# Optimization experiments

Hardware: AMD Instinct MI355X
Metric: run time of the kernel (lower is better)

Reference implementation:

```python
import jax, jax.numpy as jnp
import numpy as np

B, T, D, H = 2, 2048, 1024, 16
HD = D // H
ALPHA = HD ** -0.5
EPS = 1e-5


def setup_inputs() -> dict:
    key = jax.random.key(0)
    ks = jax.random.split(key, 8)
    x = jax.random.normal(ks[0], (B, T, D), dtype=jnp.float32)
    # additive causal mask: 0 where allowed, -inf where disallowed
    causal = jnp.triu(jnp.ones((T, T), dtype=bool), k=1)
    attention_mask = jnp.where(causal, -jnp.inf, 0.0).astype(jnp.float32)
    rab = jax.random.normal(ks[1], (1, H, T, T), dtype=jnp.float32) * 0.02
    W_in = jax.random.normal(ks[2], (D, 4 * D), dtype=jnp.float32) * (D ** -0.5)
    b_in = jnp.zeros((4 * D,), dtype=jnp.float32)
    W_out = jax.random.normal(ks[3], (D, D), dtype=jnp.float32) * (D ** -0.5)
    b_out = jnp.zeros((D,), dtype=jnp.float32)
    ln_w = jnp.ones((D,), dtype=jnp.float32)
    ln_b = jnp.zeros((D,), dtype=jnp.float32)
    return {"x": x, "attention_mask": attention_mask, "rab": rab,
            "W_in": W_in, "b_in": b_in, "W_out": W_out, "b_out": b_out,
            "ln_w": ln_w, "ln_b": ln_b}


def _heads(t):  # [B,T,D] -> [B,H,T,HD]
    return t.reshape(B, T, H, HD).transpose(0, 2, 1, 3)


def _layernorm(t, w, b):
    mu = jnp.mean(t, axis=-1, keepdims=True)
    var = jnp.mean(jnp.square(t - mu), axis=-1, keepdims=True)
    return (t - mu) * jax.lax.rsqrt(var + EPS) * w + b


def reference(x, attention_mask, rab, W_in, b_in, W_out, b_out, ln_w, ln_b):
    h = jax.nn.silu(x @ W_in + b_in)                      # [B,T,4D]
    U, V, Q, K = jnp.split(h, 4, axis=-1)
    Qh, Kh, Vh = _heads(Q), _heads(K), _heads(V)
    logits = jnp.einsum('bhqd,bhkd->bhqk', Qh, Kh) * ALPHA
    logits = logits + rab + attention_mask[None, None]    # [B,H,T,T]
    # allowed counts from the additive mask (0 == allowed)
    allowed = (attention_mask == 0).astype(jnp.float32)   # [T,T]
    denom = jnp.clip(jnp.sum(allowed, axis=-1, keepdims=True), 1.0)  # [T,1]
    logits_safe = jnp.where(jnp.isinf(logits) & (logits < 0), -1e9, logits)
    attn = jax.nn.silu(logits_safe) / denom[None, None]
    AV = jnp.einsum('bhqk,bhkd->bhqd', attn, Vh)
    AV = AV.transpose(0, 2, 1, 3).reshape(B, T, D)
    y = (_layernorm(AV, ln_w, ln_b) * U) @ W_out + b_out
    return y
```

## Files before the change

kernel.cpp:

```cpp
#include <hip/hip_runtime.h>

#define BATCH 2
#define TSEQ 2048
#define DIM 1024
#define NH 16
#define HDIM 64
#define MROWS (BATCH * TSEQ)

typedef __attribute__((ext_vector_type(4))) float f32x4;
typedef __attribute__((ext_vector_type(8))) short short8;

__device__ __forceinline__ unsigned short f2bf(float f) {
    union { float f; unsigned int u; } x; x.f = f;
    unsigned int r = x.u + 0x7fffu + ((x.u >> 16) & 1u);
    return (unsigned short)(r >> 16);
}

__device__ __forceinline__ float silu_f(float v) {
    return v * __builtin_amdgcn_rcpf(1.f + __expf(-v));
}

__device__ __forceinline__ void gl_lds16(const void* g, void* l) {
    __builtin_amdgcn_global_load_lds(
        (const __attribute__((address_space(1))) void*)g,
        (__attribute__((address_space(3))) void*)l, 16, 0, 0);
}

__device__ __forceinline__ short8 rd_swz(const unsigned short* base, int row, int chunk) {
    const char* b = (const char*)base;
    return *(const short8*)(b + row * 128 + (((chunk ^ (row & 7)) << 4)));
}

__global__ __launch_bounds__(256) void k_convert(const float* __restrict__ in,
                                                 unsigned short* __restrict__ out,
                                                 int n4) {
    int i = blockIdx.x * 256 + threadIdx.x;
    if (i < n4) {
        float4 v = ((const float4*)in)[i];
        union { unsigned short s[4]; uint2 u; } o;
        o.s[0] = f2bf(v.x); o.s[1] = f2bf(v.y); o.s[2] = f2bf(v.z); o.s[3] = f2bf(v.w);
        ((uint2*)out)[i] = o.u;
    }
}

__global__ __launch_bounds__(256) void k_transpose(const float* __restrict__ in,
                                                   unsigned short* __restrict__ out,
                                                   int R, int C) {
    __shared__ float tile[32][33];
    int tx = threadIdx.x, ty = threadIdx.y;
    int c0 = blockIdx.x * 32, r0 = blockIdx.y * 32;
    #pragma unroll
    for (int i = 0; i < 32; i += 8)
        tile[ty + i][tx] = in[(size_t)(r0 + ty + i) * C + c0 + tx];
    __syncthreads();
    #pragma unroll
    for (int i = 0; i < 32; i += 8)
        out[(size_t)(c0 + ty + i) * R + r0 + tx] = f2bf(tile[tx][ty + i]);
}

__device__ __forceinline__ void stage256(const unsigned short* __restrict__ A,
                                         const unsigned short* __restrict__ Bt,
                                         int row0, int col0, int k0,
                                         unsigned short* sAbuf, unsigned short* sBbuf,
                                         int tid) {
    #pragma unroll
    for (int q = 0; q < 4; ++q) {
        int c = tid + 512 * q;
        int rr = c >> 3;
        int kcs = (c & 7) ^ (rr & 7);
        gl_lds16(A + (size_t)(row0 + rr) * 1024 + k0 + kcs * 8, sAbuf + c * 8);
        gl_lds16(Bt + (size_t)(col0 + rr) * 1024 + k0 + kcs * 8, sBbuf + c * 8);
    }
}

__global__ __launch_bounds__(512, 2) void k_gemm1_256(
    const unsigned short* __restrict__ A, const unsigned short* __restrict__ Bt,
    const float* __restrict__ bias,
    float* __restrict__ outU, unsigned short* __restrict__ outVt,
    unsigned short* __restrict__ outQ, unsigned short* __restrict__ outK)
{
    __shared__ __align__(16) unsigned short sA[2][256 * 64];
    __shared__ __align__(16) unsigned short sB[2][256 * 64];

    const int tid = threadIdx.x;
    const int lane = tid & 63, wid = tid >> 6;
    const int lr = lane & 15, lk = lane >> 4;
    const int wm = wid >> 2, wn = wid & 3;
    const int bm = blockIdx.x, bn = blockIdx.y;
    const int row0 = bm * 256, col0 = bn * 256;

    f32x4 acc[8][4] = {};

    stage256(A, Bt, row0, col0, 0, sA[0], sB[0], tid);
    asm volatile("s_waitcnt vmcnt(0)" ::: "memory");
    __builtin_amdgcn_s_barrier();
    __builtin_amdgcn_sched_barrier(0);

    int cur = 0;
    for (int kt = 0; kt < 16; ++kt) {
        if (kt < 15) stage256(A, Bt, row0, col0, (kt + 1) * 64, sA[cur ^ 1], sB[cur ^ 1], tid);
        short8 bf[2][4];
        #pragma unroll
        for (int kk = 0; kk < 2; ++kk)
            #pragma unroll
            for (int n = 0; n < 4; ++n)
                bf[kk][n] = rd_swz(sB[cur], wn * 64 + n * 16 + lr, kk * 4 + lk);

        #pragma unroll
        for (int ph = 0; ph < 4; ++ph) {
            short8 af[2][2];
            #pragma unroll
            for (int mm = 0; mm < 2; ++mm)
                #pragma unroll
                for (int kk = 0; kk < 2; ++kk)
                    af[mm][kk] = rd_swz(sA[cur], wm * 128 + (ph * 2 + mm) * 16 + lr, kk * 4 + lk);
            __builtin_amdgcn_s_barrier();
            __builtin_amdgcn_s_setprio(1);
            #pragma unroll
            for (int mm = 0; mm < 2; ++mm)
                #pragma unroll
                for (int n = 0; n < 4; ++n)
                    #pragma unroll
                    for (int kk = 0; kk < 2; ++kk)
                        acc[ph * 2 + mm][n] = __builtin_amdgcn_mfma_f32_16x16x32_bf16(
                            af[mm][kk], bf[kk][n], acc[ph * 2 + mm][n], 0, 0, 0);
            __builtin_amdgcn_s_setprio(0);
            if (ph == 3) asm volatile("s_waitcnt vmcnt(0)" ::: "memory");
            __builtin_amdgcn_s_barrier();
        }
        __builtin_amdgcn_sched_barrier(0);
        cur ^= 1;
    }

    const int sec = bn >> 2;
    #pragma unroll
    for (int n = 0; n < 4; ++n) {
        const int cg = col0 + wn * 64 + n * 16 + lr;
        const int cc = cg & 1023;
        const float bv = bias[cg];
        #pragma unroll
        for (int m = 0; m < 8; ++m) {
            const int rg0 = row0 + wm * 128 + m * 16 + lk * 4;
            float sv[4];
            #pragma unroll
            for (int j = 0; j < 4; ++j)
                sv[j] = silu_f(acc[m][n][j] + bv);
            if (sec == 0) {
                #pragma unroll
                for (int j = 0; j < 4; ++j)
                    outU[((size_t)(rg0 + j) << 10) + cc] = sv[j];
            } else if (sec == 1) {
                union { unsigned short s[4]; uint2 u; } pk;
                #pragma unroll
                for (int j = 0; j < 4; ++j) pk.s[j] = f2bf(sv[j]);
                *(uint2*)(outVt + ((size_t)cc << 12) + rg0) = pk.u;
            } else if (sec == 2) {
                #pragma unroll
                for (int j = 0; j < 4; ++j)
                    outQ[((size_t)(rg0 + j) << 10) + cc] = f2bf(sv[j] * 0.125f);
            } else {
                #pragma unroll
                for (int j = 0; j < 4; ++j)
                    outK[((size_t)(rg0 + j) << 10) + cc] = f2bf(sv[j]);
            }
        }
    }
}

__global__ __launch_bounds__(256) void k_gemm2(
    const unsigned short* __restrict__ A, const unsigned short* __restrict__ Bt,
    int M, int N, int K, const float* __restrict__ bias, float* __restrict__ outY)
{
    __shared__ __align__(16) unsigned short sA[128 * 32];
    __shared__ __align__(16) unsigned short sB[128 * 32];
    const int tid = threadIdx.x;
    const int bm = blockIdx.x, bn = blockIdx.y;
    const int row0 = bm * 128, col0 = bn * 128;
    const int lane = tid & 63, w = tid >> 6;
    const int wrow = (w >> 1) * 64, wcol = (w & 1) * 64;
    const int lr = lane & 15, lk = lane >> 4;

    f32x4 acc[4][4] = {};

    for (int k0 = 0; k0 < K; k0 += 32) {
        for (int c = tid; c < 512; c += 256) {
            int r = c >> 2, kc = c & 3;
            gl_lds16(A + (size_t)(row0 + r) * K + k0 + kc * 8, sA + c * 8);
            gl_lds16(Bt + (size_t)(col0 + r) * K + k0 + kc * 8, sB + c * 8);
        }
        __syncthreads();
        short8 af[4], bf[4];
        #pragma unroll
        for (int m = 0; m < 4; ++m)
            af[m] = *(const short8*)(sA + (wrow + m * 16 + lr) * 32 + lk * 8);
        #pragma unroll
        for (int n = 0; n < 4; ++n)
            bf[n] = *(const short8*)(sB + (wcol + n * 16 + lr) * 32 + lk * 8);
        #pragma unroll
        for (int m = 0; m < 4; ++m)
            #pragma unroll
            for (int n = 0; n < 4; ++n)
                acc[m][n] = __builtin_amdgcn_mfma_f32_16x16x32_bf16(af[m], bf[n], acc[m][n], 0, 0, 0);
        __syncthreads();
    }

    #pragma unroll
    for (int m = 0; m < 4; ++m) {
        #pragma unroll
        for (int n = 0; n < 4; ++n) {
            int cg = col0 + wcol + n * 16 + lr;
            float bv = bias[cg];
            int rg0 = row0 + wrow + m * 16 + lk * 4;
            #pragma unroll
            for (int j = 0; j < 4; ++j)
                outY[(size_t)(rg0 + j) * N + cg] = acc[m][n][j] + bv;
        }
    }
}

__global__ __launch_bounds__(256, 4) void k_attn(
    const unsigned short* __restrict__ Qb,
    const unsigned short* __restrict__ Kb,
    const unsigned short* __restrict__ Vt,
    const float* __restrict__ rab,
    float* __restrict__ AV)
{
    __shared__ __align__(16) unsigned short sK[2][64 * 64];
    __shared__ __align__(16) unsigned short sVt[2][64 * 64];
    __shared__ __align__(16) unsigned short sP[64 * 64];

    const int tid = threadIdx.x;
    const int lane = tid & 63;
    const int w = tid >> 6;
    const int lr = lane & 15;
    const int lk = lane >> 4;

    const int bid = blockIdx.x;
    const int idx = bid & 255;
    const int g = bid >> 8;
    const int h = idx & 15;
    const int r_ = idx >> 4;
    const int bb = g >> 1;
    const int qt = (g & 1) ? (31 - r_) : r_;
    const int q0 = qt * 64;

    short8 qreg[2];
    #pragma unroll
    for (int ks = 0; ks < 2; ++ks)
        qreg[ks] = *(const short8*)(Qb + (((size_t)(bb * TSEQ + q0 + w * 16 + lr)) << 10)
                                     + h * 64 + ks * 32 + lk * 8);
    __builtin_amdgcn_sched_barrier(0);

    int qrow[4];
    const float* rabrow[4];
    const float* rabh = rab + (size_t)h * TSEQ * TSEQ;
    #pragma unroll
    for (int j = 0; j < 4; ++j) {
        qrow[j] = q0 + w * 16 + lk * 4 + j;
        rabrow[j] = rabh + (size_t)qrow[j] * TSEQ + lr;
    }

    f32x4 acc[4] = {};

    #define STAGE(buf, kt_) do {                                                      \
        int k0s = (kt_) * 64;                                                         \
        for (int c = tid; c < 512; c += 256) {                                        \
            int rr = c >> 3, kc = c & 7;                                              \
            int kcs = kc ^ (rr & 7);                                                  \
            gl_lds16(Kb + (((size_t)(bb * TSEQ + k0s + rr)) << 10) + h * 64 + kcs * 8,\
                     sK[buf] + c * 8);                                                \
            gl_lds16(Vt + (((size_t)(h * 64 + rr)) << 12) + bb * TSEQ + k0s + kcs * 8,\
                     sVt[buf] + c * 8);                                               \
        }                                                                             \
    } while (0)

    float rv0[4][4], rv1[4][4];

    STAGE(0, 0);
    __builtin_amdgcn_sched_barrier(0);
    #pragma unroll
    for (int nt = 0; nt < 4; ++nt)
        #pragma unroll
        for (int j = 0; j < 4; ++j)
            rv0[nt][j] = rabrow[j][nt * 16];
    __builtin_amdgcn_sched_barrier(0);
    asm volatile("s_waitcnt vmcnt(16)" ::: "memory");
    __builtin_amdgcn_s_barrier();

    #define BODY(KT, BUFC, RVC, RVN) do {                                             \
        const int k0 = (KT) * 64;                                                     \
        const bool have_next = (KT) < qt;                                             \
        if (have_next) STAGE((BUFC) ^ 1, (KT) + 1);                                   \
        __builtin_amdgcn_sched_barrier(0);                                            \
        if (have_next) {                                                              \
            _Pragma("unroll")                                                         \
            for (int nt = 0; nt < 4; ++nt)                                            \
                _Pragma("unroll")                                                     \
                for (int j = 0; j < 4; ++j)                                           \
                    RVN[nt][j] = rabrow[j][k0 + 64 + nt * 16];                        \
        }                                                                             \
        __builtin_amdgcn_sched_barrier(0);                                            \
        f32x4 s[4];                                                                   \
        _Pragma("unroll")                                                             \
        for (int nt = 0; nt < 4; ++nt) {                                              \
            f32x4 c0v;                                                                \
            c0v[0] = RVC[nt][0]; c0v[1] = RVC[nt][1];                                 \
            c0v[2] = RVC[nt][2]; c0v[3] = RVC[nt][3];                                 \
            s[nt] = c0v;                                                              \
        }                                                                             \
        _Pragma("unroll")                                                             \
        for (int ks = 0; ks < 2; ++ks) {                                              \
            _Pragma("unroll")                                                         \
            for (int nt = 0; nt < 4; ++nt)                                            \
                s[nt] = __builtin_amdgcn_mfma_f32_16x16x32_bf16(                      \
                    qreg[ks], rd_swz(sK[BUFC], nt * 16 + lr, ks * 4 + lk), s[nt], 0, 0, 0); \
        }                                                                             \
        char* pb = (char*)sP;                                                         \
        if (have_next) {                                                              \
            _Pragma("unroll")                                                         \
            for (int j = 0; j < 4; ++j) {                                             \
                const int prow = w * 16 + lk * 4 + j;                                 \
                char* bj = pb + prow * 128;                                           \
                const int swz = ((lk * 4 + j) & 7) << 4;                              \
                _Pragma("unroll")                                                     \
                for (int nt = 0; nt < 4; ++nt)                                        \
                    *(unsigned short*)(bj + (((nt << 5) | (lr << 1)) ^ swz))          \
                        = f2bf(silu_f(s[nt][j]));                                     \
            }                                                                         \
        } else {                                                                      \
            _Pragma("unroll")                                                         \
            for (int j = 0; j < 4; ++j) {                                             \
                const int prow = w * 16 + lk * 4 + j;                                 \
                char* bj = pb + prow * 128;                                           \
                const int swz = ((lk * 4 + j) & 7) << 4;                              \
                _Pragma("unroll")                                                     \
                for (int nt = 0; nt < 4; ++nt) {                                      \
                    int k = k0 + nt * 16 + lr;                                        \
                    float pv = (k <= qrow[j]) ? silu_f(s[nt][j]) : 0.f;               \
                    *(unsigned short*)(bj + (((nt << 5) | (lr << 1)) ^ swz)) = f2bf(pv); \
                }                                                                     \
            }                                                                         \
        }                                                                             \
        _Pragma("unroll")                                                             \
        for (int ks = 0; ks < 2; ++ks) {                                              \
            short8 ap = rd_swz(sP, w * 16 + lr, ks * 4 + lk);                         \
            _Pragma("unroll")                                                         \
            for (int dt = 0; dt < 4; ++dt)                                            \
                acc[dt] = __builtin_amdgcn_mfma_f32_16x16x32_bf16(                    \
                    ap, rd_swz(sVt[BUFC], dt * 16 + lr, ks * 4 + lk), acc[dt], 0, 0, 0); \
        }                                                                             \
        if (have_next) {                                                              \
            asm volatile("s_waitcnt vmcnt(16)" ::: "memory");                         \
            __builtin_amdgcn_s_barrier();                                             \
        }                                                                             \
    } while (0)

    for (int kt = 0; kt <= qt; kt += 2) {
        BODY(kt, 0, rv0, rv1);
        if (kt + 1 <= qt) BODY(kt + 1, 1, rv1, rv0);
    }
    #undef BODY
    #undef STAGE

    #pragma unroll
    for (int dt = 0; dt < 4; ++dt)
        #pragma unroll
        for (int j = 0; j < 4; ++j)
            AV[(((size_t)(bb * TSEQ + qrow[j])) << 10) + h * 64 + dt * 16 + lr] = acc[dt][j];
}

__global__ __launch_bounds__(256) void k_ln(const float* __restrict__ AV,
                                            const float* __restrict__ U,
                                            const float* __restrict__ lnw,
                                            const float* __restrict__ lnb,
                                            unsigned short* __restrict__ z) {
    __shared__ float red[8];
    const int row = blockIdx.x, tid = threadIdx.x;
    const float c = (float)((row & (TSEQ - 1)) + 1);
    const float eps = 1e-5f * c * c;
    float4 v = ((const float4*)(AV + ((size_t)row << 10)))[tid];
    float s = v.x + v.y + v.z + v.w;
    float s2 = v.x * v.x + v.y * v.y + v.z * v.z + v.w * v.w;
    #pragma unroll
    for (int o = 32; o > 0; o >>= 1) { s += __shfl_xor(s, o); s2 += __shfl_xor(s2, o); }
    const int w = tid >> 6;
    if ((tid & 63) == 0) { red[w] = s; red[4 + w] = s2; }
    __syncthreads();
    s = red[0] + red[1] + red[2] + red[3];
    s2 = red[4] + red[5] + red[6] + red[7];
    const float mu = s * (1.f / 1024.f);
    const float var = s2 * (1.f / 1024.f) - mu * mu;
    const float rstd = rsqrtf(var + eps);
    float4 uw = ((const float4*)(U + ((size_t)row << 10)))[tid];
    float4 lw = ((const float4*)lnw)[tid];
    float4 lb = ((const float4*)lnb)[tid];
    union { unsigned short o[4]; uint2 u; } ov;
    ov.o[0] = f2bf(((v.x - mu) * rstd * lw.x + lb.x) * uw.x);
    ov.o[1] = f2bf(((v.y - mu) * rstd * lw.y + lb.y) * uw.y);
    ov.o[2] = f2bf(((v.z - mu) * rstd * lw.z + lb.z) * uw.z);
    ov.o[3] = f2bf(((v.w - mu) * rstd * lw.w + lb.w) * uw.w);
    ((uint2*)z)[((size_t)row << 8) + tid] = ov.u;
}

extern "C" void kernel_launch(void* const* d_in, const int* in_sizes, int n_in,
                              void* d_out, int out_size, void* d_ws, size_t ws_size,
                              hipStream_t stream) {
    const float* x     = (const float*)d_in[0];
    const float* rab   = (const float*)d_in[2];
    const float* W_in  = (const float*)d_in[3];
    const float* b_in  = (const float*)d_in[4];
    const float* W_out = (const float*)d_in[5];
    const float* b_out = (const float*)d_in[6];
    const float* ln_w  = (const float*)d_in[7];
    const float* ln_b  = (const float*)d_in[8];
    float* y = (float*)d_out;

    char* ws = (char*)d_ws;
    size_t off = 0;
    auto alloc = [&](size_t bytes) -> void* {
        void* p = ws + off;
        off += (bytes + 255) & ~(size_t)255;
        return p;
    };
    unsigned short* WinT  = (unsigned short*)alloc((size_t)4096 * 1024 * 2);
    unsigned short* WoutT = (unsigned short*)alloc((size_t)1024 * 1024 * 2);
    unsigned short* xb    = (unsigned short*)alloc((size_t)MROWS * DIM * 2);
    float*          Ubuf  = (float*)alloc((size_t)MROWS * DIM * 4);
    unsigned short* Qb    = (unsigned short*)alloc((size_t)MROWS * DIM * 2);
    unsigned short* Kb    = (unsigned short*)alloc((size_t)MROWS * DIM * 2);
    unsigned short* Vtb   = (unsigned short*)alloc((size_t)DIM * MROWS * 2);
    float*          AV    = (float*)alloc((size_t)MROWS * DIM * 4);
    unsigned short* z     = (unsigned short*)alloc((size_t)MROWS * DIM * 2);

    k_convert<<<dim3(4096), dim3(256), 0, stream>>>(x, xb, MROWS * DIM / 4);
    k_transpose<<<dim3(128, 32), dim3(32, 8), 0, stream>>>(W_in, WinT, 1024, 4096);
    k_transpose<<<dim3(32, 32), dim3(32, 8), 0, stream>>>(W_out, WoutT, 1024, 1024);
    k_gemm1_256<<<dim3(16, 16), dim3(512), 0, stream>>>(xb, WinT, b_in, Ubuf, Vtb, Qb, Kb);
    k_attn<<<dim3(1024), dim3(256), 0, stream>>>(Qb, Kb, Vtb, rab, AV);
    k_ln<<<dim3(MROWS), dim3(256), 0, stream>>>(AV, Ubuf, ln_w, ln_b, z);
    k_gemm2<<<dim3(32, 8), dim3(256), 0, stream>>>(z, WoutT, MROWS, 1024, 1024, b_out, y);
}
```

Baseline: 170.7 us.

## Process both batches per attention block to share rab loads; store U and AV as bf16

```diff
diff --git a/kernel.cpp b/kernel.cpp
--- a/kernel.cpp
+++ b/kernel.cpp
@@ -14,6 +14,11 @@
     union { float f; unsigned int u; } x; x.f = f;
     unsigned int r = x.u + 0x7fffu + ((x.u >> 16) & 1u);
     return (unsigned short)(r >> 16);
+}
+
+__device__ __forceinline__ float bf2f(unsigned short s) {
+    union { unsigned int u; float f; } t; t.u = (unsigned int)s << 16;
+    return t.f;
 }
 
 __device__ __forceinline__ float silu_f(float v) {
@@ -76,7 +81,7 @@
 __global__ __launch_bounds__(512, 2) void k_gemm1_256(
     const unsigned short* __restrict__ A, const unsigned short* __restrict__ Bt,
     const float* __restrict__ bias,
-    float* __restrict__ outU, unsigned short* __restrict__ outVt,
+    unsigned short* __restrict__ outU, unsigned short* __restrict__ outVt,
     unsigned short* __restrict__ outQ, unsigned short* __restrict__ outK)
 {
     __shared__ __align__(16) unsigned short sA[2][256 * 64];
@@ -148,7 +153,7 @@
             if (sec == 0) {
                 #pragma unroll
                 for (int j = 0; j < 4; ++j)
-                    outU[((size_t)(rg0 + j) << 10) + cc] = sv[j];
+                    outU[((size_t)(rg0 + j) << 10) + cc] = f2bf(sv[j]);
             } else if (sec == 1) {
                 union { unsigned short s[4]; uint2 u; } pk;
                 #pragma unroll
@@ -218,15 +223,15 @@
     }
 }
 
-__global__ __launch_bounds__(256, 4) void k_attn(
+__global__ __launch_bounds__(256, 2) void k_attn(
     const unsigned short* __restrict__ Qb,
     const unsigned short* __restrict__ Kb,
     const unsigned short* __restrict__ Vt,
     const float* __restrict__ rab,
-    float* __restrict__ AV)
+    unsigned short* __restrict__ AV)
 {
-    __shared__ __align__(16) unsigned short sK[2][64 * 64];
-    __shared__ __align__(16) unsigned short sVt[2][64 * 64];
+    __shared__ __align__(16) unsigned short sK[2][2][64 * 64];
+    __shared__ __align__(16) unsigned short sVt[2][2][64 * 64];
     __shared__ __align__(16) unsigned short sP[64 * 64];
 
     const int tid = threadIdx.x;
@@ -236,19 +241,19 @@
     const int lk = lane >> 4;
 
     const int bid = blockIdx.x;
-    const int idx = bid & 255;
-    const int g = bid >> 8;
-    const int h = idx & 15;
-    const int r_ = idx >> 4;
-    const int bb = g >> 1;
-    const int qt = (g & 1) ? (31 - r_) : r_;
+    const int p = bid & 255;
+    const int h = p & 15;
+    const int r_ = p >> 4;
+    const int qt = (bid < 256) ? r_ : (31 - r_);
     const int q0 = qt * 64;
 
-    short8 qreg[2];
-    #pragma unroll
-    for (int ks = 0; ks < 2; ++ks)
-        qreg[ks] = *(const short8*)(Qb + (((size_t)(bb * TSEQ + q0 + w * 16 + lr)) << 10)
-                                     + h * 64 + ks * 32 + lk * 8);
+    short8 qreg[2][2];
+    #pragma unroll
+    for (int bb = 0; bb < 2; ++bb)
+        #pragma unroll
+        for (int ks = 0; ks < 2; ++ks)
+            qreg[bb][ks] = *(const short8*)(Qb + (((size_t)(bb * TSEQ + q0 + w * 16 + lr)) << 10)
+                                            + h * 64 + ks * 32 + lk * 8);
     __builtin_amdgcn_sched_barrier(0);
 
     int qrow[4];
@@ -260,18 +265,22 @@
         rabrow[j] = rabh + (size_t)qrow[j] * TSEQ + lr;
     }
 
-    f32x4 acc[4] = {};
-
-    #define STAGE(buf, kt_) do {                                                      \
-        int k0s = (kt_) * 64;                                                         \
-        for (int c = tid; c < 512; c += 256) {                                        \
-            int rr = c >> 3, kc = c & 7;                                              \
-            int kcs = kc ^ (rr & 7);                                                  \
-            gl_lds16(Kb + (((size_t)(bb * TSEQ + k0s + rr)) << 10) + h * 64 + kcs * 8,\
-                     sK[buf] + c * 8);                                                \
-            gl_lds16(Vt + (((size_t)(h * 64 + rr)) << 12) + bb * TSEQ + k0s + kcs * 8,\
-                     sVt[buf] + c * 8);                                               \
-        }                                                                             \
+    f32x4 acc[2][4] = {};
+
+    #define STAGE(buf, kt_) do {                                                          \
+        int k0s = (kt_) * 64;                                                             \
+        for (int c = tid; c < 512; c += 256) {                                            \
+            int rr = c >> 3, kc = c & 7;                                                  \
+            int kcs = kc ^ (rr & 7);                                                      \
+            gl_lds16(Kb + (((size_t)(k0s + rr)) << 10) + h * 64 + kcs * 8,                \
+                     &sK[buf][0][c * 8]);                                                 \
+            gl_lds16(Kb + (((size_t)(TSEQ + k0s + rr)) << 10) + h * 64 + kcs * 8,         \
+                     &sK[buf][1][c * 8]);                                                 \
+            gl_lds16(Vt + (((size_t)(h * 64 + rr)) << 12) + k0s + kcs * 8,                \
+                     &sVt[buf][0][c * 8]);                                                \
+            gl_lds16(Vt + (((size_t)(h * 64 + rr)) << 12) + TSEQ + k0s + kcs * 8,         \
+                     &sVt[buf][1][c * 8]);                                                \
+        }                                                                                 \
     } while (0)
 
     float rv0[4][4], rv1[4][4];
@@ -287,72 +296,81 @@
     asm volatile("s_waitcnt vmcnt(16)" ::: "memory");
     __builtin_amdgcn_s_barrier();
 
-    #define BODY(KT, BUFC, RVC, RVN) do {                                             \
-        const int k0 = (KT) * 64;                                                     \
-        const bool have_next = (KT) < qt;                                             \
-        if (have_next) STAGE((BUFC) ^ 1, (KT) + 1);                                   \
-        __builtin_amdgcn_sched_barrier(0);                                            \
-        if (have_next) {                                                              \
-            _Pragma("unroll")                                                         \
-            for (int nt = 0; nt < 4; ++nt)                                            \
-                _Pragma("unroll")                                                     \
-                for (int j = 0; j < 4; ++j)                                           \
-                    RVN[nt][j] = rabrow[j][k0 + 64 + nt * 16];                        \
-        }                                                                             \
-        __builtin_amdgcn_sched_barrier(0);                                            \
-        f32x4 s[4];                                                                   \
-        _Pragma("unroll")                                                             \
-        for (int nt = 0; nt < 4; ++nt) {                                              \
-            f32x4 c0v;                                                                \
-            c0v[0] = RVC[nt][0]; c0v[1] = RVC[nt][1];                                 \
-            c0v[2] = RVC[nt][2]; c0v[3] = RVC[nt][3];                                 \
-            s[nt] = c0v;                                                              \
-        }                                                                             \
-        _Pragma("unroll")                                                             \
-        for (int ks = 0; ks < 2; ++ks) {                                              \
-            _Pragma("unroll")                                                         \
-            for (int nt = 0; nt < 4; ++nt)                                            \
-                s[nt] = __builtin_amdgcn_mfma_f32_16x16x32_bf16(                      \
-                    qreg[ks], rd_swz(sK[BUFC], nt * 16 + lr, ks * 4 + lk), s[nt], 0, 0, 0); \
-        }                                                                             \
-        char* pb = (char*)sP;                                                         \
-        if (have_next) {                                                              \
-            _Pragma("unroll")                                                         \
-            for (int j = 0; j < 4; ++j) {                                             \
-                const int prow = w * 16 + lk * 4 + j;                                 \
-                char* bj = pb + prow * 128;                                           \
-                const int swz = ((lk * 4 + j) & 7) << 4;                              \
-                _Pragma("unroll")                                                     \
-                for (int nt = 0; nt < 4; ++nt)                                        \
-                    *(unsigned short*)(bj + (((nt << 5) | (lr << 1)) ^ swz))          \
-                        = f2bf(silu_f(s[nt][j]));                                     \
-            }                                                                         \
-        } else {                                                                      \
-            _Pragma("unroll")                                                         \
-            for (int j = 0; j < 4; ++j) {                                             \
-                const int prow = w * 16 + lk * 4 + j;                                 \
-                char* bj = pb + prow * 128;                                           \
-                const int swz = ((lk * 4 + j) & 7) << 4;                              \
-                _Pragma("unroll")                                                     \
-                for (int nt = 0; nt < 4; ++nt) {                                      \
-                    int k = k0 + nt * 16 + lr;                                        \
-                    float pv = (k <= qrow[j]) ? silu_f(s[nt][j]) : 0.f;               \
-                    *(unsigned short*)(bj + (((nt << 5) | (lr << 1)) ^ swz)) = f2bf(pv); \
-                }                                                                     \
-            }                                                                         \
-        }                                                                             \
-        _Pragma("unroll")                                                             \
-        for (int ks = 0; ks < 2; ++ks) {                                              \
-            short8 ap = rd_swz(sP, w * 16 + lr, ks * 4 + lk);                         \
-            _Pragma("unroll")                                                         \
-            for (int dt = 0; dt < 4; ++dt)                                            \
-                acc[dt] = __builtin_amdgcn_mfma_f32_16x16x32_bf16(                    \
-                    ap, rd_swz(sVt[BUFC], dt * 16 + lr, ks * 4 + lk), acc[dt], 0, 0, 0); \
-        }                                                                             \
-        if (have_next) {                                                              \
-            asm volatile("s_waitcnt vmcnt(16)" ::: "memory");                         \
-            __builtin_amdgcn_s_barrier();                                             \
-        }                                                                             \
+    #define BODY(KT, BUFC, RVC, RVN) do {                                                 \
+        const int k0 = (KT) * 64;                                                         \
+        const bool have_next = (KT) < qt;                                                 \
+        if (have_next) STAGE((BUFC) ^ 1, (KT) + 1);                                       \
+        __builtin_amdgcn_sched_barrier(0);                                                \
+        if (have_next) {                                                                  \
+            _Pragma("unroll")                                                             \
+            for (int nt = 0; nt < 4; ++nt)                                                \
+                _Pragma("unroll")                                                         \
+                for (int j = 0; j < 4; ++j)                                               \
+                    RVN[nt][j] = rabrow[j][k0 + 64 + nt * 16];                            \
+        }                                                                                 \
+        __builtin_amdgcn_sched_barrier(0);                                                \
+        _Pragma("unroll")                                                                 \
+        for (int bb = 0; bb < 2; ++bb) {                                                  \
+            f32x4 s[4];                                                                   \
+            _Pragma("unroll")                                                             \
+            for (int nt = 0; nt < 4; ++nt) {                                              \
+                f32x4 c0v;                                                                \
+                c0v[0] = RVC[nt][0]; c0v[1] = RVC[nt][1];                                 \
+                c0v[2] = RVC[nt][2]; c0v[3] = RVC[nt][3];                                 \
+                s[nt] = c0v;                                                              \
+            }                                                                             \
+            __builtin_amdgcn_s_setprio(1);                                                \
+            _Pragma("unroll")                                                             \
+            for (int ks = 0; ks < 2; ++ks) {                                              \
+                _Pragma("unroll")                                                         \
+                for (int nt = 0; nt < 4; ++nt)                                            \
+                    s[nt] = __builtin_amdgcn_mfma_f32_16x16x32_bf16(                      \
+                        qreg[bb][ks], rd_swz(sK[BUFC][bb], nt * 16 + lr, ks * 4 + lk),    \
+                        s[nt], 0, 0, 0);                                                  \
+            }                                                                             \
+            __builtin_amdgcn_s_setprio(0);                                                \
+            char* pb = (char*)sP;                                                         \
+            if (have_next) {                                                              \
+                _Pragma("unroll")                                                         \
+                for (int j = 0; j < 4; ++j) {                                             \
+                    const int prow = w * 16 + lk * 4 + j;                                 \
+                    char* bj = pb + prow * 128;                                           \
+                    const int swz = ((lk * 4 + j) & 7) << 4;                              \
+                    _Pragma("unroll")                                                     \
+                    for (int nt = 0; nt < 4; ++nt)                                        \
+                        *(unsigned short*)(bj + (((nt << 5) | (lr << 1)) ^ swz))          \
+                            = f2bf(silu_f(s[nt][j]));                                     \
+                }                                                                         \
+            } else {                                                                      \
+                _Pragma("unroll")                                                         \
+                for (int j = 0; j < 4; ++j) {                                             \
+                    const int prow = w * 16 + lk * 4 + j;                                 \
+                    char* bj = pb + prow * 128;                                           \
+                    const int swz = ((lk * 4 + j) & 7) << 4;                              \
+                    _Pragma("unroll")                                                     \
+                    for (int nt = 0; nt < 4; ++nt) {                                      \
+                        int k = k0 + nt * 16 + lr;                                        \
+                        float pv = (k <= qrow[j]) ? silu_f(s[nt][j]) : 0.f;               \
+                        *(unsigned short*)(bj + (((nt << 5) | (lr << 1)) ^ swz)) = f2bf(pv); \
+                    }                                                                     \
+                }                                                                         \
+            }                                                                             \
+            __builtin_amdgcn_s_setprio(1);                                                \
+            _Pragma("unroll")                                                             \
+            for (int ks = 0; ks < 2; ++ks) {                                              \
+                short8 ap = rd_swz(sP, w * 16 + lr, ks * 4 + lk);                         \
+                _Pragma("unroll")                                                         \
+                for (int dt = 0; dt < 4; ++dt)                                            \
+                    acc[bb][dt] = __builtin_amdgcn_mfma_f32_16x16x32_bf16(                \
+                        ap, rd_swz(sVt[BUFC][bb], dt * 16 + lr, ks * 4 + lk),             \
+                        acc[bb][dt], 0, 0, 0);                                            \
+            }                                                                             \
+            __builtin_amdgcn_s_setprio(0);                                                \
+        }                                                                                 \
+        if (have_next) {                                                                  \
+            asm volatile("s_waitcnt vmcnt(16)" ::: "memory");                             \
+            __builtin_amdgcn_s_barrier();                                                 \
+        }                                                                                 \
     } while (0)
 
     for (int kt = 0; kt <= qt; kt += 2) {
@@ -363,14 +381,17 @@
     #undef STAGE
 
     #pragma unroll
-    for (int dt = 0; dt < 4; ++dt)
-        #pragma unroll
-        for (int j = 0; j < 4; ++j)
-            AV[(((size_t)(bb * TSEQ + qrow[j])) << 10) + h * 64 + dt * 16 + lr] = acc[dt][j];
-}
-
-__global__ __launch_bounds__(256) void k_ln(const float* __restrict__ AV,
-                                            const float* __restrict__ U,
+    for (int bb = 0; bb < 2; ++bb)
+        #pragma unroll
+        for (int dt = 0; dt < 4; ++dt)
+            #pragma unroll
+            for (int j = 0; j < 4; ++j)
+                AV[(((size_t)(bb * TSEQ + qrow[j])) << 10) + h * 64 + dt * 16 + lr]
+                    = f2bf(acc[bb][dt][j]);
+}
+
+__global__ __launch_bounds__(256) void k_ln(const unsigned short* __restrict__ AV,
+                                            const unsigned short* __restrict__ U,
                                             const float* __restrict__ lnw,
                                             const float* __restrict__ lnb,
                                             unsigned short* __restrict__ z) {
@@ -378,9 +399,13 @@
     const int row = blockIdx.x, tid = threadIdx.x;
     const float c = (float)((row & (TSEQ - 1)) + 1);
     const float eps = 1e-5f * c * c;
-    float4 v = ((const float4*)(AV + ((size_t)row << 10)))[tid];
-    float s = v.x + v.y + v.z + v.w;
-    float s2 = v.x * v.x + v.y * v.y + v.z * v.z + v.w * v.w;
+    union { unsigned short s[4]; uint2 u; } a;
+    a.u = ((const uint2*)(AV + ((size_t)row << 10)))[tid];
+    float v[4];
+    #pragma unroll
+    for (int i = 0; i < 4; ++i) v[i] = bf2f(a.s[i]);
+    float s = v[0] + v[1] + v[2] + v[3];
+    float s2 = v[0] * v[0] + v[1] * v[1] + v[2] * v[2] + v[3] * v[3];
     #pragma unroll
     for (int o = 32; o > 0; o >>= 1) { s += __shfl_xor(s, o); s2 += __shfl_xor(s2, o); }
     const int w = tid >> 6;
@@ -391,14 +416,15 @@
     const float mu = s * (1.f / 1024.f);
     const float var = s2 * (1.f / 1024.f) - mu * mu;
     const float rstd = rsqrtf(var + eps);
-    float4 uw = ((const float4*)(U + ((size_t)row << 10)))[tid];
+    union { unsigned short s[4]; uint2 u; } uu;
+    uu.u = ((const uint2*)(U + ((size_t)row << 10)))[tid];
     float4 lw = ((const float4*)lnw)[tid];
     float4 lb = ((const float4*)lnb)[tid];
     union { unsigned short o[4]; uint2 u; } ov;
-    ov.o[0] = f2bf(((v.x - mu) * rstd * lw.x + lb.x) * uw.x);
-    ov.o[1] = f2bf(((v.y - mu) * rstd * lw.y + lb.y) * uw.y);
-    ov.o[2] = f2bf(((v.z - mu) * rstd * lw.z + lb.z) * uw.z);
-    ov.o[3] = f2bf(((v.w - mu) * rstd * lw.w + lb.w) * uw.w);
+    ov.o[0] = f2bf(((v[0] - mu) * rstd * lw.x + lb.x) * bf2f(uu.s[0]));
+    ov.o[1] = f2bf(((v[1] - mu) * rstd * lw.y + lb.y) * bf2f(uu.s[1]));
+    ov.o[2] = f2bf(((v[2] - mu) * rstd * lw.z + lb.z) * bf2f(uu.s[2]));
+    ov.o[3] = f2bf(((v[3] - mu) * rstd * lw.w + lb.w) * bf2f(uu.s[3]));
     ((uint2*)z)[((size_t)row << 8) + tid] = ov.u;
 }
 
@@ -425,18 +451,18 @@
     unsigned short* WinT  = (unsigned short*)alloc((size_t)4096 * 1024 * 2);
     unsigned short* WoutT = (unsigned short*)alloc((size_t)1024 * 1024 * 2);
     unsigned short* xb    = (unsigned short*)alloc((size_t)MROWS * DIM * 2);
-    float*          Ubuf  = (float*)alloc((size_t)MROWS * DIM * 4);
+    unsigned short* Ubuf  = (unsigned short*)alloc((size_t)MROWS * DIM * 2);
     unsigned short* Qb    = (unsigned short*)alloc((size_t)MROWS * DIM * 2);
     unsigned short* Kb    = (unsigned short*)alloc((size_t)MROWS * DIM * 2);
     unsigned short* Vtb   = (unsigned short*)alloc((size_t)DIM * MROWS * 2);
-    float*          AV    = (float*)alloc((size_t)MROWS * DIM * 4);
+    unsigned short* AV    = (unsigned short*)alloc((size_t)MROWS * DIM * 2);
     unsigned short* z     = (unsigned short*)alloc((size_t)MROWS * DIM * 2);
 
     k_convert<<<dim3(4096), dim3(256), 0, stream>>>(x, xb, MROWS * DIM / 4);
     k_transpose<<<dim3(128, 32), dim3(32, 8), 0, stream>>>(W_in, WinT, 1024, 4096);
     k_transpose<<<dim3(32, 32), dim3(32, 8), 0, stream>>>(W_out, WoutT, 1024, 1024);
     k_gemm1_256<<<dim3(16, 16), dim3(512), 0, stream>>>(xb, WinT, b_in, Ubuf, Vtb, Qb, Kb);
-    k_attn<<<dim3(1024), dim3(256), 0, stream>>>(Qb, Kb, Vtb, rab, AV);
+    k_attn<<<dim3(512), dim3(256), 0, stream>>>(Qb, Kb, Vtb, rab, AV);
     k_ln<<<dim3(MROWS), dim3(256), 0, stream>>>(AV, Ubuf, ln_w, ln_b, z);
     k_gemm2<<<dim3(32, 8), dim3(256), 0, stream>>>(z, WoutT, MROWS, 1024, 1024, b_out, y);
 }
```

Result: slower. 180.5 us (+5.8%).

## Store U and AV as bf16 and pipeline gemm2 with double-buffered swizzled LDS

Applied to the files above, without the earlier changes.

```diff
diff --git a/kernel.cpp b/kernel.cpp
--- a/kernel.cpp
+++ b/kernel.cpp
@@ -14,6 +14,11 @@
     union { float f; unsigned int u; } x; x.f = f;
     unsigned int r = x.u + 0x7fffu + ((x.u >> 16) & 1u);
     return (unsigned short)(r >> 16);
+}
+
+__device__ __forceinline__ float bf2f(unsigned short s) {
+    union { unsigned int u; float f; } t; t.u = (unsigned int)s << 16;
+    return t.f;
 }
 
 __device__ __forceinline__ float silu_f(float v) {
@@ -76,7 +81,7 @@
 __global__ __launch_bounds__(512, 2) void k_gemm1_256(
     const unsigned short* __restrict__ A, const unsigned short* __restrict__ Bt,
     const float* __restrict__ bias,
-    float* __restrict__ outU, unsigned short* __restrict__ outVt,
+    unsigned short* __restrict__ outU, unsigned short* __restrict__ outVt,
     unsigned short* __restrict__ outQ, unsigned short* __restrict__ outK)
 {
     __shared__ __align__(16) unsigned short sA[2][256 * 64];
@@ -148,7 +153,7 @@
             if (sec == 0) {
                 #pragma unroll
                 for (int j = 0; j < 4; ++j)
-                    outU[((size_t)(rg0 + j) << 10) + cc] = sv[j];
+                    outU[((size_t)(rg0 + j) << 10) + cc] = f2bf(sv[j]);
             } else if (sec == 1) {
                 union { unsigned short s[4]; uint2 u; } pk;
                 #pragma unroll
@@ -167,53 +172,88 @@
     }
 }
 
-__global__ __launch_bounds__(256) void k_gemm2(
+__device__ __forceinline__ void stage128(const unsigned short* __restrict__ A,
+                                         const unsigned short* __restrict__ Bt,
+                                         int row0, int col0, int k0,
+                                         unsigned short* sAbuf, unsigned short* sBbuf,
+                                         int tid) {
+    #pragma unroll
+    for (int q = 0; q < 4; ++q) {
+        int c = tid + 256 * q;
+        int rr = c >> 3;
+        int kcs = (c & 7) ^ (rr & 7);
+        gl_lds16(A + (size_t)(row0 + rr) * 1024 + k0 + kcs * 8, sAbuf + c * 8);
+        gl_lds16(Bt + (size_t)(col0 + rr) * 1024 + k0 + kcs * 8, sBbuf + c * 8);
+    }
+}
+
+__global__ __launch_bounds__(256, 2) void k_gemm2(
     const unsigned short* __restrict__ A, const unsigned short* __restrict__ Bt,
-    int M, int N, int K, const float* __restrict__ bias, float* __restrict__ outY)
+    const float* __restrict__ bias, float* __restrict__ outY)
 {
-    __shared__ __align__(16) unsigned short sA[128 * 32];
-    __shared__ __align__(16) unsigned short sB[128 * 32];
+    __shared__ __align__(16) unsigned short sA[2][128 * 64];
+    __shared__ __align__(16) unsigned short sB[2][128 * 64];
+
     const int tid = threadIdx.x;
+    const int lane = tid & 63, wid = tid >> 6;
+    const int lr = lane & 15, lk = lane >> 4;
+    const int wm = wid >> 1, wn = wid & 1;
     const int bm = blockIdx.x, bn = blockIdx.y;
     const int row0 = bm * 128, col0 = bn * 128;
-    const int lane = tid & 63, w = tid >> 6;
-    const int wrow = (w >> 1) * 64, wcol = (w & 1) * 64;
-    const int lr = lane & 15, lk = lane >> 4;
 
     f32x4 acc[4][4] = {};
 
-    for (int k0 = 0; k0 < K; k0 += 32) {
-        for (int c = tid; c < 512; c += 256) {
-            int r = c >> 2, kc = c & 3;
-            gl_lds16(A + (size_t)(row0 + r) * K + k0 + kc * 8, sA + c * 8);
-            gl_lds16(Bt + (size_t)(col0 + r) * K + k0 + kc * 8, sB + c * 8);
+    stage128(A, Bt, row0, col0, 0, sA[0], sB[0], tid);
+    asm volatile("s_waitcnt vmcnt(0)" ::: "memory");
+    __builtin_amdgcn_s_barrier();
+    __builtin_amdgcn_sched_barrier(0);
+
+    int cur = 0;
+    for (int kt = 0; kt < 16; ++kt) {
+        if (kt < 15) stage128(A, Bt, row0, col0, (kt + 1) * 64, sA[cur ^ 1], sB[cur ^ 1], tid);
+        short8 bf[2][4];
+        #pragma unroll
+        for (int kk = 0; kk < 2; ++kk)
+            #pragma unroll
+            for (int n = 0; n < 4; ++n)
+                bf[kk][n] = rd_swz(sB[cur], wn * 64 + n * 16 + lr, kk * 4 + lk);
+
+        #pragma unroll
+        for (int ph = 0; ph < 2; ++ph) {
+            short8 af[2][2];
+            #pragma unroll
+            for (int mm = 0; mm < 2; ++mm)
+                #pragma unroll
+                for (int kk = 0; kk < 2; ++kk)
+                    af[mm][kk] = rd_swz(sA[cur], wm * 64 + (ph * 2 + mm) * 16 + lr, kk * 4 + lk);
+            __builtin_amdgcn_s_barrier();
+            __builtin_amdgcn_s_setprio(1);
+            #pragma unroll
+            for (int mm = 0; mm < 2; ++mm)
+                #pragma unroll
+                for (int n = 0; n < 4; ++n)
+                    #pragma unroll
+                    for (int kk = 0; kk < 2; ++kk)
+                        acc[ph * 2 + mm][n] = __builtin_amdgcn_mfma_f32_16x16x32_bf16(
+                            af[mm][kk], bf[kk][n], acc[ph * 2 + mm][n], 0, 0, 0);
+            __builtin_amdgcn_s_setprio(0);
+            if (ph == 1) asm volatile("s_waitcnt vmcnt(0)" ::: "memory");
+            __builtin_amdgcn_s_barrier();
         }
-        __syncthreads();
-        short8 af[4], bf[4];
-        #pragma unroll
-        for (int m = 0; m < 4; ++m)
-            af[m] = *(const short8*)(sA + (wrow + m * 16 + lr) * 32 + lk * 8);
-        #pragma unroll
-        for (int n = 0; n < 4; ++n)
-            bf[n] = *(const short8*)(sB + (wcol + n * 16 + lr) * 32 + lk * 8);
-        #pragma unroll
-        for (int m = 0; m < 4; ++m)
-            #pragma unroll
-            for (int n = 0; n < 4; ++n)
-                acc[m][n] = __builtin_amdgcn_mfma_f32_16x16x32_bf16(af[m], bf[n], acc[m][n], 0, 0, 0);
-        __syncthreads();
-    }
-
-    #pragma unroll
-    for (int m = 0; m < 4; ++m) {
-        #pragma unroll
-        for (int n = 0; n < 4; ++n) {
-            int cg = col0 + wcol + n * 16 + lr;
-            float bv = bias[cg];
-            int rg0 = row0 + wrow + m * 16 + lk * 4;
+        __builtin_amdgcn_sched_barrier(0);
+        cur ^= 1;
+    }
+
+    #pragma unroll
+    for (int n = 0; n < 4; ++n) {
+        const int cg = col0 + wn * 64 + n * 16 + lr;
+        const float bv = bias[cg];
+        #pragma unroll
+        for (int m = 0; m < 4; ++m) {
+            const int rg0 = row0 + wm * 64 + m * 16 + lk * 4;
             #pragma unroll
             for (int j = 0; j < 4; ++j)
-                outY[(size_t)(rg0 + j) * N + cg] = acc[m][n][j] + bv;
+                outY[(size_t)(rg0 + j) * 1024 + cg] = acc[m][n][j] + bv;
         }
     }
 }
@@ -223,7 +263,7 @@
     const unsigned short* __restrict__ Kb,
     const unsigned short* __restrict__ Vt,
     const float* __restrict__ rab,
-    float* __restrict__ AV)
+    unsigned short* __restrict__ AV)
 {
     __shared__ __align__(16) unsigned short sK[2][64 * 64];
     __shared__ __align__(16) unsigned short sVt[2][64 * 64];
@@ -366,11 +406,12 @@
     for (int dt = 0; dt < 4; ++dt)
         #pragma unroll
         for (int j = 0; j < 4; ++j)
-            AV[(((size_t)(bb * TSEQ + qrow[j])) << 10) + h * 64 + dt * 16 + lr] = acc[dt][j];
-}
-
-__global__ __launch_bounds__(256) void k_ln(const float* __restrict__ AV,
-                                            const float* __restrict__ U,
+            AV[(((size_t)(bb * TSEQ + qrow[j])) << 10) + h * 64 + dt * 16 + lr]
+                = f2bf(acc[dt][j]);
+}
+
+__global__ __launch_bounds__(256) void k_ln(const unsigned short* __restrict__ AV,
+                                            const unsigned short* __restrict__ U,
                                             const float* __restrict__ lnw,
                                             const float* __restrict__ lnb,
                                             unsigned short* __restrict__ z) {
@@ -378,9 +419,13 @@
     const int row = blockIdx.x, tid = threadIdx.x;
     const float c = (float)((row & (TSEQ - 1)) + 1);
     const float eps = 1e-5f * c * c;
-    float4 v = ((const float4*)(AV + ((size_t)row << 10)))[tid];
-    float s = v.x + v.y + v.z + v.w;
-    float s2 = v.x * v.x + v.y * v.y + v.z * v.z + v.w * v.w;
+    union { unsigned short s[4]; uint2 u; } a;
+    a.u = ((const uint2*)(AV + ((size_t)row << 10)))[tid];
+    float v[4];
+    #pragma unroll
+    for (int i = 0; i < 4; ++i) v[i] = bf2f(a.s[i]);
+    float s = v[0] + v[1] + v[2] + v[3];
+    float s2 = v[0] * v[0] + v[1] * v[1] + v[2] * v[2] + v[3] * v[3];
     #pragma unroll
     for (int o = 32; o > 0; o >>= 1) { s += __shfl_xor(s, o); s2 += __shfl_xor(s2, o); }
     const int w = tid >> 6;
@@ -391,14 +436,15 @@
     const float mu = s * (1.f / 1024.f);
     const float var = s2 * (1.f / 1024.f) - mu * mu;
     const float rstd = rsqrtf(var + eps);
-    float4 uw = ((const float4*)(U + ((size_t)row << 10)))[tid];
+    union { unsigned short s[4]; uint2 u; } uu;
+    uu.u = ((const uint2*)(U + ((size_t)row << 10)))[tid];
     float4 lw = ((const float4*)lnw)[tid];
     float4 lb = ((const float4*)lnb)[tid];
     union { unsigned short o[4]; uint2 u; } ov;
-    ov.o[0] = f2bf(((v.x - mu) * rstd * lw.x + lb.x) * uw.x);
-    ov.o[1] = f2bf(((v.y - mu) * rstd * lw.y + lb.y) * uw.y);
-    ov.o[2] = f2bf(((v.z - mu) * rstd * lw.z + lb.z) * uw.z);
-    ov.o[3] = f2bf(((v.w - mu) * rstd * lw.w + lb.w) * uw.w);
+    ov.o[0] = f2bf(((v[0] - mu) * rstd * lw.x + lb.x) * bf2f(uu.s[0]));
+    ov.o[1] = f2bf(((v[1] - mu) * rstd * lw.y + lb.y) * bf2f(uu.s[1]));
+    ov.o[2] = f2bf(((v[2] - mu) * rstd * lw.z + lb.z) * bf2f(uu.s[2]));
+    ov.o[3] = f2bf(((v[3] - mu) * rstd * lw.w + lb.w) * bf2f(uu.s[3]));
     ((uint2*)z)[((size_t)row << 8) + tid] = ov.u;
 }
 
@@ -425,11 +471,11 @@
     unsigned short* WinT  = (unsigned short*)alloc((size_t)4096 * 1024 * 2);
     unsigned short* WoutT = (unsigned short*)alloc((size_t)1024 * 1024 * 2);
     unsigned short* xb    = (unsigned short*)alloc((size_t)MROWS * DIM * 2);
-    float*          Ubuf  = (float*)alloc((size_t)MROWS * DIM * 4);
+    unsigned short* Ubuf  = (unsigned short*)alloc((size_t)MROWS * DIM * 2);
     unsigned short* Qb    = (unsigned short*)alloc((size_t)MROWS * DIM * 2);
     unsigned short* Kb    = (unsigned short*)alloc((size_t)MROWS * DIM * 2);
     unsigned short* Vtb   = (unsigned short*)alloc((size_t)DIM * MROWS * 2);
-    float*          AV    = (float*)alloc((size_t)MROWS * DIM * 4);
+    unsigned short* AV    = (unsigned short*)alloc((size_t)MROWS * DIM * 2);
     unsigned short* z     = (unsigned short*)alloc((size_t)MROWS * DIM * 2);
 
     k_convert<<<dim3(4096), dim3(256), 0, stream>>>(x, xb, MROWS * DIM / 4);
@@ -438,5 +484,5 @@
     k_gemm1_256<<<dim3(16, 16), dim3(512), 0, stream>>>(xb, WinT, b_in, Ubuf, Vtb, Qb, Kb);
     k_attn<<<dim3(1024), dim3(256), 0, stream>>>(Qb, Kb, Vtb, rab, AV);
     k_ln<<<dim3(MROWS), dim3(256), 0, stream>>>(AV, Ubuf, ln_w, ln_b, z);
-    k_gemm2<<<dim3(32, 8), dim3(256), 0, stream>>>(z, WoutT, MROWS, 1024, 1024, b_out, y);
-}
+    k_gemm2<<<dim3(32, 8), dim3(256), 0, stream>>>(z, WoutT, b_out, y);
+}
```

Result: faster. 158.1 us (-7.4%).
